# Kernel optimization log

Hardware: AMD Instinct MI355X
Metric: run time of the kernel (lower is better)

Reference implementation:

```python
import jax, jax.numpy as jnp
import numpy as np

NUM_HEADS = 12

def _attn(q, k, v, scale):
    # q,k,v: [..., L, hd]; softmax attention over L (key axis)
    s = jnp.einsum('...qd,...kd->...qk', q, k) * scale
    a = jax.nn.softmax(s, axis=-1)
    return jnp.einsum('...qk,...kd->...qd', a, v)

def setup_inputs() -> dict:
    key = jax.random.key(0)
    k1, k2, k3 = jax.random.split(key, 3)
    B, N, C, D = 8, 256, 16, 768
    x = jax.random.normal(k1, (B, N, C, D), dtype=jnp.float32)
    w_qkv = jax.random.normal(k2, (D, 6 * D), dtype=jnp.float32) * (D ** -0.5)
    w_proj = jax.random.normal(k3, (D, D), dtype=jnp.float32) * (D ** -0.5)
    b_proj = jnp.zeros((D,), dtype=jnp.float32)
    return {"x": x, "w_qkv": w_qkv, "w_proj": w_proj, "b_proj": b_proj}

def reference(x, w_qkv, w_proj, b_proj):
    B, N, C, D = x.shape
    H = NUM_HEADS
    hd = D // H
    scale = hd ** -0.5
    # qkv: [B,N,C,6,H,hd] -> [6,B,H,N,C,hd]
    qkv = (x @ w_qkv).reshape(B, N, C, 6, H, hd).transpose(3, 0, 4, 1, 2, 5)
    qc, kc, qs, ks, vc, vs = qkv[0], qkv[1], qkv[2], qkv[3], qkv[4], qkv[5]
    # spatial attention over N (per channel c): move to [B,H,C,N,hd]
    qs = jnp.swapaxes(qs, -2, -3)
    ks = jnp.swapaxes(ks, -2, -3)
    vs = jnp.swapaxes(vs, -2, -3)
    xs = _attn(qs, ks, vs, scale)          # [B,H,C,N,hd]
    xs = jnp.swapaxes(xs, -2, -3)          # [B,H,N,C,hd]
    # channel attention over C (per token n)
    xc = _attn(qc, kc, vc, scale)          # [B,H,N,C,hd]
    out = xs * xc                           # elementwise combine (fused path)
    # matches torch: x.transpose(1,2).reshape(B,N,C,D)
    out = out.transpose(0, 2, 1, 3, 4).reshape(B, N, C, D)
    return out @ w_proj + b_proj
```

## Files before the change

### kernel.cpp

```cpp
#include <hip/hip_runtime.h>

typedef _Float16 f16;
typedef f16  f16x8 __attribute__((ext_vector_type(8)));
typedef float f32x4 __attribute__((ext_vector_type(4)));

#define S3 3145728LL

__device__ __forceinline__ f32x4 mm(f16x8 a, f16x8 b, f32x4 c) {
  return __builtin_amdgcn_mfma_f32_16x16x32_f16(a, b, c, 0, 0, 0);
}
__device__ __forceinline__ void BAR() { asm volatile("s_barrier" ::: "memory"); }

__device__ __forceinline__ int esw(int t, int col) {
  return t * 128 + ((((col >> 3) ^ ((t ^ (t >> 3)) & 7)) << 3) | (col & 7));
}
__device__ __forceinline__ int oesw(int t, int col) {
  return t * 64 + ((((col >> 3) ^ (t & 7)) << 3) | (col & 7));
}

__global__ void cvt_T_kernel(const float* __restrict__ in, f16* __restrict__ out,
                             int R, int Cc) {
  __shared__ float tile[32][33];
  int tc = blockIdx.x, tr = blockIdx.y;
  int lr = threadIdx.x & 31, lw = threadIdx.x >> 5;
  int c0 = tc * 32, r0 = tr * 32;
#pragma unroll
  for (int i = 0; i < 4; i++)
    tile[lw + 8 * i][lr] = in[(size_t)(r0 + lw + 8 * i) * Cc + c0 + lr];
  __syncthreads();
#pragma unroll
  for (int i = 0; i < 4; i++)
    out[(size_t)(c0 + lw + 8 * i) * R + r0 + lr] = (f16)tile[lr][lw + 8 * i];
}

__global__ void cvt_x_kernel(const float* __restrict__ in, f16* __restrict__ out) {
  size_t i = ((size_t)blockIdx.x * 256 + threadIdx.x) * 8;
  f32x4 a = __builtin_nontemporal_load((const f32x4*)(in + i));
  f32x4 b = __builtin_nontemporal_load((const f32x4*)(in + i + 4));
  f16x8 o;
#pragma unroll
  for (int j = 0; j < 4; j++) { o[j] = (f16)a[j]; o[4 + j] = (f16)b[j]; }
  *(f16x8*)(out + i) = o;
}

#define QST_A(c, q, kt) __builtin_amdgcn_global_load_lds( \
    (const __attribute__((address_space(1))) void*)(aSrc + (size_t)(q) * 24576 + (size_t)(kt) * 64), \
    (__attribute__((address_space(3))) void*)((char*)lds + (c) * 32768 + (q) * 1024 * 4 + wave * 1024), 16, 0, 0)
#define QST_B(c, q, kt) __builtin_amdgcn_global_load_lds( \
    (const __attribute__((address_space(1))) void*)(bSrc + (size_t)(q) * 24576 + (size_t)(kt) * 64), \
    (__attribute__((address_space(3))) void*)((char*)lds + 16384 + (c) * 32768 + (q) * 1024 * 4 + wave * 1024), 16, 0, 0)

__global__ __launch_bounds__(256, 2) void gemm_qkvT(
    const f16* __restrict__ A, const f16* __restrict__ Bt,
    f16* __restrict__ area, long long cstr_) {
  __shared__ f16 lds[32768];
  size_t cstr = (size_t)cstr_;
  int id  = blockIdx.x;
  int cpx = gridDim.x >> 3;
  int id2 = (id & 7) * cpx + (id >> 3);
  int sr = id2 / 288, rr = id2 % 288;
  int bm = sr * 8 + (rr & 7), bn = rr >> 3;

  int tid = threadIdx.x;
  int wave = tid >> 6, lane = tid & 63;
  int l16 = lane & 15, lq = lane >> 4;
  int wr = wave >> 1, wc = wave & 1;
  int l7 = l16 & 7;
  int cb0 = ((lq) ^ l7) << 4;
  int cb1 = ((4 + lq) ^ l7) << 4;

  const f16* aSrc = A  + (size_t)(bm * 128 + (tid >> 3)) * 768 +
                    (((tid & 7) ^ ((tid >> 3) & 7)) << 3);
  const f16* bSrc = Bt + (size_t)(bn * 128 + (tid >> 3)) * 768 +
                    (((tid & 7) ^ ((tid >> 3) & 7)) << 3);

  f32x4 zz = {0.f, 0.f, 0.f, 0.f};
  f32x4 acc[4][4];
#pragma unroll
  for (int m = 0; m < 4; m++)
#pragma unroll
    for (int n = 0; n < 4; n++) acc[m][n] = zz;

#pragma unroll
  for (int q = 0; q < 4; q++) { QST_A(0, q, 0); }
#pragma unroll
  for (int q = 0; q < 4; q++) { QST_B(0, q, 0); }
#pragma unroll
  for (int q = 0; q < 4; q++) { QST_A(1, q, 1); }
#pragma unroll
  for (int q = 0; q < 4; q++) { QST_B(1, q, 1); }
  asm volatile("s_waitcnt vmcnt(8)" ::: "memory");
  BAR();

  f16x8 af[4][2], bf[4][2];
#pragma unroll 2
  for (int t = 0; t < 12; ++t) {
    int c = t & 1;
    const char* ab = (const char*)lds + c * 32768;
    const char* bb = ab + 16384;
    int rA = wr * 64 + l16;
    int rB = wc * 64 + l16;
#pragma unroll
    for (int mf = 0; mf < 4; mf++) {
      af[mf][0] = *(const f16x8*)(ab + (rA + mf * 16) * 128 + cb0);
      af[mf][1] = *(const f16x8*)(ab + (rA + mf * 16) * 128 + cb1);
    }
#pragma unroll
    for (int nf = 0; nf < 4; nf++) {
      bf[nf][0] = *(const f16x8*)(bb + (rB + nf * 16) * 128 + cb0);
      bf[nf][1] = *(const f16x8*)(bb + (rB + nf * 16) * 128 + cb1);
    }
    asm volatile("s_waitcnt lgkmcnt(0)" ::: "memory");
    BAR();
    if (t < 10) {
#pragma unroll
      for (int q = 0; q < 4; q++) { QST_A(c, q, t + 2); }
#pragma unroll
      for (int q = 0; q < 4; q++) { QST_B(c, q, t + 2); }
    }
    __builtin_amdgcn_s_setprio(1);
#pragma unroll
    for (int ks = 0; ks < 2; ks++)
#pragma unroll
      for (int mf = 0; mf < 4; mf++)
#pragma unroll
        for (int nf = 0; nf < 4; nf++)
          acc[mf][nf] = mm(af[mf][ks], bf[nf][ks], acc[mf][nf]);
    __builtin_amdgcn_s_setprio(0);
    if (t < 10) asm volatile("s_waitcnt vmcnt(8)" ::: "memory");
    else        asm volatile("s_waitcnt vmcnt(0)" ::: "memory");
    BAR();
  }

  int s  = bn / 6;
  int h0 = (bn % 6) * 2;
  size_t comp;
  if (s == 0) comp = 0; else if (s == 1) comp = 1; else if (s == 2) comp = 3;
  else if (s == 3) comp = 4; else if (s == 4) comp = 2; else comp = 5;
  int g = (bm * 128) >> 12;
  size_t base = comp * cstr + (size_t)g * S3;
  int n0 = (bm & 31) * 8;

  __syncthreads();
#pragma unroll
  for (int mi = 0; mi < 4; mi++)
#pragma unroll
    for (int ni = 0; ni < 4; ni++)
#pragma unroll
      for (int r = 0; r < 4; r++) {
        int t = wr * 64 + mi * 16 + lq * 4 + r;
        int col = wc * 64 + ni * 16 + l16;
        lds[esw(t, col)] = (f16)acc[mi][ni][r];
      }
  __syncthreads();

  if (s < 2) {
#pragma unroll
    for (int i = 0; i < 4; i++) {
      int u = wave * 4 + i;
      int hl = u >> 3, j16 = u & 7;
#pragma unroll
      for (int half = 0; half < 2; half++) {
        int e0 = half * 512 + lane * 8;
        int cc = e0 >> 6, d0 = e0 & 63;
        f16x8 v = *(const f16x8*)&lds[esw(j16 * 16 + cc, hl * 64 + d0)];
        __builtin_nontemporal_store(v, (f16x8*)&area[base +
            (size_t)(h0 + hl) * 262144 + (size_t)(n0 + j16) * 1024 + e0]);
      }
    }
  } else if (s < 4) {
#pragma unroll
    for (int i = 0; i < 8; i++) {
      int u = wave * 8 + i;
      int hl = u >> 4, cc = u & 15;
      int e = lane * 8;
      int nl = e >> 6, d0 = e & 63;
      f16x8 v = *(const f16x8*)&lds[esw(nl * 16 + cc, hl * 64 + d0)];
      __builtin_nontemporal_store(v, (f16x8*)&area[base +
          (size_t)((h0 + hl) * 16 + cc) * 16384 + (size_t)n0 * 64 + e]);
    }
  } else if (s == 4) {
#pragma unroll
    for (int i = 0; i < 4; i++) {
      int u = wave * 4 + i;
      int hl = u >> 3, j8 = u & 7;
#pragma unroll
      for (int half = 0; half < 2; half++) {
        int e0 = half * 512 + lane * 8;
        int d0 = e0 >> 4, cb = e0 & 15;
        f16x8 v;
#pragma unroll
        for (int j = 0; j < 8; j++)
          v[j] = lds[esw(j8 * 16 + cb + j, hl * 64 + d0)];
        __builtin_nontemporal_store(v, (f16x8*)&area[base +
            (size_t)((h0 + hl) * 256 + n0 + j8) * 1024 + e0]);
      }
    }
  } else {
#pragma unroll
    for (int i = 0; i < 8; i++) {
      int u = wave * 8 + i;
      int hl = u >> 4, cc = u & 15;
      int e = lane * 8;
      int d0 = e >> 3;
      f16x8 v;
#pragma unroll
      for (int j = 0; j < 8; j++)
        v[j] = lds[esw(j * 16 + cc, hl * 64 + d0)];
      __builtin_nontemporal_store(v, (f16x8*)&area[base +
          ((size_t)((h0 + hl) * 16 + cc) * 32 + (bm & 31)) * 512 + e]);
    }
  }
}

__global__ __launch_bounds__(256, 2) void gemm_projT(
    const f16* __restrict__ A,
    const f16* __restrict__ Bt,
    const float* __restrict__ bias, float* __restrict__ Cout) {
  __shared__ f16 lds[32768];
  int id  = blockIdx.x;
  int cpx = gridDim.x >> 3;
  int id2 = (id & 7) * cpx + (id >> 3);
  int sr = id2 / 48, rr = id2 % 48;
  int bm = sr * 8 + (rr & 7), bn = rr >> 3;

  int tid = threadIdx.x;
  int wave = tid >> 6, lane = tid & 63;
  int l16 = lane & 15, lq = lane >> 4;
  int wr = wave >> 1, wc = wave & 1;
  int l7 = l16 & 7;
  int cb0 = ((lq) ^ l7) << 4;
  int cb1 = ((4 + lq) ^ l7) << 4;

  const f16* aSrc = A  + (size_t)(bm * 128 + (tid >> 3)) * 768 +
                    (((tid & 7) ^ ((tid >> 3) & 7)) << 3);
  const f16* bSrc = Bt + (size_t)(bn * 128 + (tid >> 3)) * 768 +
                    (((tid & 7) ^ ((tid >> 3) & 7)) << 3);

  f32x4 zz = {0.f, 0.f, 0.f, 0.f};
  f32x4 acc[4][4];
#pragma unroll
  for (int m = 0; m < 4; m++)
#pragma unroll
    for (int n = 0; n < 4; n++) acc[m][n] = zz;

#pragma unroll
  for (int q = 0; q < 4; q++) { QST_A(0, q, 0); }
#pragma unroll
  for (int q = 0; q < 4; q++) { QST_B(0, q, 0); }
#pragma unroll
  for (int q = 0; q < 4; q++) { QST_A(1, q, 1); }
#pragma unroll
  for (int q = 0; q < 4; q++) { QST_B(1, q, 1); }
  asm volatile("s_waitcnt vmcnt(8)" ::: "memory");
  BAR();

  f16x8 af[4][2], bf[4][2];
#pragma unroll 2
  for (int t = 0; t < 12; ++t) {
    int c = t & 1;
    const char* ab = (const char*)lds + c * 32768;
    const char* bb = ab + 16384;
    int rA = wr * 64 + l16;
    int rB = wc * 64 + l16;
#pragma unroll
    for (int mf = 0; mf < 4; mf++) {
      af[mf][0] = *(const f16x8*)(ab + (rA + mf * 16) * 128 + cb0);
      af[mf][1] = *(const f16x8*)(ab + (rA + mf * 16) * 128 + cb1);
    }
#pragma unroll
    for (int nf = 0; nf < 4; nf++) {
      bf[nf][0] = *(const f16x8*)(bb + (rB + nf * 16) * 128 + cb0);
      bf[nf][1] = *(const f16x8*)(bb + (rB + nf * 16) * 128 + cb1);
    }
    asm volatile("s_waitcnt lgkmcnt(0)" ::: "memory");
    BAR();
    if (t < 10) {
#pragma unroll
      for (int q = 0; q < 4; q++) { QST_A(c, q, t + 2); }
#pragma unroll
      for (int q = 0; q < 4; q++) { QST_B(c, q, t + 2); }
    }
    __builtin_amdgcn_s_setprio(1);
#pragma unroll
    for (int ks = 0; ks < 2; ks++)
#pragma unroll
      for (int mf = 0; mf < 4; mf++)
#pragma unroll
        for (int nf = 0; nf < 4; nf++)
          acc[mf][nf] = mm(af[mf][ks], bf[nf][ks], acc[mf][nf]);
    __builtin_amdgcn_s_setprio(0);
    if (t < 10) asm volatile("s_waitcnt vmcnt(8)" ::: "memory");
    else        asm volatile("s_waitcnt vmcnt(0)" ::: "memory");
    BAR();
  }

#pragma unroll
  for (int ni = 0; ni < 4; ni++) {
    int col = bn * 128 + wc * 64 + ni * 16 + l16;
    float bb = bias[col];
#pragma unroll
    for (int mi = 0; mi < 4; mi++) {
#pragma unroll
      for (int r = 0; r < 4; r++) {
        int row = bm * 128 + wr * 64 + mi * 16 + lq * 4 + r;
        __builtin_nontemporal_store(acc[mi][ni][r] + bb,
                                    &Cout[(size_t)row * 768 + col]);
      }
    }
  }
}

__global__ __launch_bounds__(512) void attn_spat_kernel(f16* __restrict__ area,
                                                        long long cstr_) {
  size_t cstr = (size_t)cstr_;
  int blk = blockIdx.x;
  int g = blk / 192, rem = blk % 192;
  int h = rem >> 4, c = rem & 15;
  size_t goff = (size_t)g * S3;
  const f16* qs = area + 3 * cstr + goff + (size_t)((h * 16 + c) * 256) * 64;
  const f16* ks = area + 4 * cstr + goff + (size_t)((h * 16 + c) * 256) * 64;
  const f16* vsb = area + 5 * cstr + goff + (size_t)(h * 16 + c) * 16384;
  f16* xsn = area + 6 * cstr + goff;

  int tid = threadIdx.x;
  int wave = tid >> 6, lane = tid & 63;
  int l16 = lane & 15, lq = lane >> 4;
  __shared__ f16 plds[8][32][40];
  __shared__ f16 osm[16384];

  f32x4 zz = {0.f, 0.f, 0.f, 0.f};
  f16x8 aq[2][2];
#pragma unroll
  for (int m = 0; m < 2; m++)
#pragma unroll
    for (int kd = 0; kd < 2; kd++)
      aq[m][kd] = *(const f16x8*)&qs[(size_t)(wave * 32 + m * 16 + l16) * 64 + kd * 32 + lq * 8];

  f32x4 o[2][4];
  float mrow[2][4], lrow[2][4];
#pragma unroll
  for (int m = 0; m < 2; m++) {
#pragma unroll
    for (int n = 0; n < 4; n++) o[m][n] = zz;
#pragma unroll
    for (int r = 0; r < 4; r++) { mrow[m][r] = -1e30f; lrow[m][r] = 0.f; }
  }

  for (int kc = 0; kc < 8; kc++) {
    int k0 = kc * 32;
    f16x8 bk00 = *(const f16x8*)&ks[(size_t)(k0 + l16) * 64 + lq * 8];
    f16x8 bk01 = *(const f16x8*)&ks[(size_t)(k0 + l16) * 64 + 32 + lq * 8];
    f16x8 bk10 = *(const f16x8*)&ks[(size_t)(k0 + 16 + l16) * 64 + lq * 8];
    f16x8 bk11 = *(const f16x8*)&ks[(size_t)(k0 + 16 + l16) * 64 + 32 + lq * 8];
    f32x4 st[2][2];
#pragma unroll
    for (int m = 0; m < 2; m++) {
      st[m][0] = mm(aq[m][1], bk01, mm(aq[m][0], bk00, zz));
      st[m][1] = mm(aq[m][1], bk11, mm(aq[m][0], bk10, zz));
    }
#pragma unroll
    for (int m = 0; m < 2; m++) {
#pragma unroll
      for (int r = 0; r < 4; r++) {
        float s0 = st[m][0][r] * 0.125f, s1 = st[m][1][r] * 0.125f;
        float t = fmaxf(s0, s1);
        t = fmaxf(t, __shfl_xor(t, 1));
        t = fmaxf(t, __shfl_xor(t, 2));
        t = fmaxf(t, __shfl_xor(t, 4));
        t = fmaxf(t, __shfl_xor(t, 8));
        float mold = mrow[m][r];
        float mnew = fmaxf(mold, t);
        float fac  = __expf(mold - mnew);
        mrow[m][r] = mnew;
        float p0 = __expf(s0 - mnew), p1 = __expf(s1 - mnew);
        lrow[m][r] = lrow[m][r] * fac + p0 + p1;
        o[m][0][r] *= fac; o[m][1][r] *= fac; o[m][2][r] *= fac; o[m][3][r] *= fac;
        int prow = m * 16 + lq * 4 + r;
        plds[wave][prow][l16]      = (f16)p0;
        plds[wave][prow][16 + l16] = (f16)p1;
      }
    }
    f16x8 ap0 = *(const f16x8*)&plds[wave][l16][lq * 8];
    f16x8 ap1 = *(const f16x8*)&plds[wave][16 + l16][lq * 8];
#pragma unroll
    for (int n = 0; n < 4; n++) {
      f16x8 bv = *(const f16x8*)&vsb[((k0 >> 3) + lq) * 512 + (n * 16 + l16) * 8];
      o[0][n] = mm(ap0, bv, o[0][n]);
      o[1][n] = mm(ap1, bv, o[1][n]);
    }
  }
#pragma unroll
  for (int m = 0; m < 2; m++)
#pragma unroll
    for (int r = 0; r < 4; r++) {
      float l = lrow[m][r];
      l += __shfl_xor(l, 1);
      l += __shfl_xor(l, 2);
      l += __shfl_xor(l, 4);
      l += __shfl_xor(l, 8);
      lrow[m][r] = 1.0f / l;
    }
#pragma unroll
  for (int m = 0; m < 2; m++)
#pragma unroll
    for (int n = 0; n < 4; n++)
#pragma unroll
      for (int r = 0; r < 4; r++) {
        int row = wave * 32 + m * 16 + lq * 4 + r;
        osm[oesw(row, n * 16 + l16)] = (f16)(o[m][n][r] * lrow[m][r]);
      }
  __syncthreads();
  size_t hc64 = (size_t)(h * 16 + c) * 64;
#pragma unroll
  for (int i = 0; i < 4; i++) {
    int row = i * 64 + (tid >> 3);
    int dp  = (tid & 7) * 8;
    f16x8 v = *(const f16x8*)&osm[oesw(row, dp)];
    __builtin_nontemporal_store(v, (f16x8*)&xsn[(size_t)row * 12288 + hc64 + dp]);
  }
}

__global__ __launch_bounds__(256) void attn_chan_kernel(f16* __restrict__ area,
                                                        long long cstr_) {
  size_t cstr = (size_t)cstr_;
  int blk = blockIdx.x;
  int g = blk >> 8, n = blk & 255;
  size_t goff = (size_t)g * S3;
  int tid = threadIdx.x;
  int wave = tid >> 6, lane = tid & 63;
  int l16 = lane & 15, lq = lane >> 4;
  __shared__ f16 xsl[12288];
  __shared__ f16 prl[12288];
  __shared__ f16 plds[4][16][40];

  const f16* xsn = area + 6 * cstr + goff + (size_t)n * 12288;
#pragma unroll
  for (int i = 0; i < 6; i++) {
    int seg = wave * 6 + i;
    __builtin_amdgcn_global_load_lds(
        (const __attribute__((address_space(1))) void*)(xsn + seg * 512 + lane * 8),
        (__attribute__((address_space(3))) void*)((char*)xsl + seg * 1024), 16, 0, 0);
  }
  if (lane < 16) {
#pragma unroll
    for (int j = 0; j < 16; j++) plds[wave][lane][16 + j] = (f16)0.f;
  }
  asm volatile("s_waitcnt vmcnt(0)" ::: "memory");
  __syncthreads();

  f32x4 zz = {0.f, 0.f, 0.f, 0.f};
  for (int hi = 0; hi < 3; hi++) {
    int h = wave + hi * 4;
    const f16* q = area + 0 * cstr + goff + (size_t)((h * 256 + n) * 16) * 64;
    const f16* k = area + 1 * cstr + goff + (size_t)((h * 256 + n) * 16) * 64;
    const f16* v = area + 2 * cstr + goff + (size_t)((h * 256 + n) * 64) * 16;
    f16x8 a0 = *(const f16x8*)&q[l16 * 64 + lq * 8];
    f16x8 a1 = *(const f16x8*)&q[l16 * 64 + 32 + lq * 8];
    f16x8 b0 = *(const f16x8*)&k[l16 * 64 + lq * 8];
    f16x8 b1 = *(const f16x8*)&k[l16 * 64 + 32 + lq * 8];
    f32x4 s = mm(a1, b1, mm(a0, b0, zz));
    float p[4];
#pragma unroll
    for (int r = 0; r < 4; r++) {
      float t = s[r] * 0.125f;
      float mx = t;
      mx = fmaxf(mx, __shfl_xor(mx, 1));
      mx = fmaxf(mx, __shfl_xor(mx, 2));
      mx = fmaxf(mx, __shfl_xor(mx, 4));
      mx = fmaxf(mx, __shfl_xor(mx, 8));
      float e = __expf(t - mx);
      float sum = e;
      sum += __shfl_xor(sum, 1);
      sum += __shfl_xor(sum, 2);
      sum += __shfl_xor(sum, 4);
      sum += __shfl_xor(sum, 8);
      p[r] = e / sum;
    }
#pragma unroll
    for (int r = 0; r < 4; r++)
      plds[wave][lq * 4 + r][l16] = (f16)p[r];
    f16x8 ap = *(const f16x8*)&plds[wave][l16][lq * 8];
#pragma unroll
    for (int nt = 0; nt < 4; nt++) {
      f16x8 bv = *(const f16x8*)&v[(nt * 16 + l16) * 16 + lq * 8];
      f32x4 o = mm(ap, bv, zz);
#pragma unroll
      for (int r = 0; r < 4; r++) {
        int cq = lq * 4 + r, d = nt * 16 + l16;
        int idx = h * 1024 + cq * 64 + d;
        float xsv = (float)xsl[idx];
        prl[idx] = (f16)(o[r] * xsv);
      }
    }
  }
  __syncthreads();
  f16* prod = area + 3 * cstr + goff + (size_t)n * 12288;
#pragma unroll
  for (int i = 0; i < 6; i++) {
    f16x8 v = *(const f16x8*)&prl[i * 2048 + tid * 8];
    __builtin_nontemporal_store(v, (f16x8*)&prod[i * 2048 + tid * 8]);
  }
}

extern "C" void kernel_launch(void* const* d_in, const int* in_sizes, int n_in,
                              void* d_out, int out_size, void* d_ws, size_t ws_size,
                              hipStream_t stream) {
  const float* x      = (const float*)d_in[0];
  const float* w_qkv  = (const float*)d_in[1];
  const float* w_proj = (const float*)d_in[2];
  const float* b_proj = (const float*)d_in[3];
  float* out = (float*)d_out;
  f16* ws = (f16*)d_ws;

  const size_t W16T = 4608ull * 768;
  const size_t WPT  = 768ull * 768;
  f16* w16t = ws;
  f16* wpt  = ws + W16T;
  f16* area = wpt + WPT;

  int G = 8;
  while (G > 1 && (W16T + WPT + 7ull * G * S3) * 2 > ws_size) G >>= 1;
  int nch = 8 / G;
  long long cstr = (long long)G * S3;
  f16* x16 = area + 6 * (size_t)cstr;

  cvt_T_kernel<<<dim3(144, 24), 256, 0, stream>>>(w_qkv, w16t, 768, 4608);
  cvt_T_kernel<<<dim3(24, 24), 256, 0, stream>>>(w_proj, wpt, 768, 768);

  for (int ch = 0; ch < nch; ch++) {
    size_t b0 = (size_t)ch * G;
    cvt_x_kernel<<<G * 1536, 256, 0, stream>>>(x + b0 * S3, x16);
    gemm_qkvT<<<G * 1152, 256, 0, stream>>>(x16, w16t, area, cstr);
    attn_spat_kernel<<<G * 192, 512, 0, stream>>>(area, cstr);
    attn_chan_kernel<<<G * 256, 256, 0, stream>>>(area, cstr);
    gemm_projT<<<G * 192, 256, 0, stream>>>(area + 3 * (size_t)cstr, wpt, b_proj,
                                            out + b0 * S3);
  }
}
```

Baseline: 508.2 us.

## Replace QKV GEMM with 256x256-tile, 8-wave, four-phase pipelined kernel

The QKV projection GEMM moves from 128x128 tiles with 4 waves to 256x256 tiles with 8 waves and 128 KB of LDS double buffering. The K-loop is split into four MFMA phases, and the global-to-LDS loads for the next stages are interleaved between them. The aim is more reuse of each loaded tile and better overlap of loads with MFMA work. The scatter epilogue is unified for the larger tile, at the cost of fewer workgroups and more LDS and register pressure per block.

Result: no change. 504.1 us (-0.8%).

```diff
diff --git a/kernel.cpp b/kernel.cpp
--- a/kernel.cpp
+++ b/kernel.cpp
@@ -10,9 +10,11 @@
   return __builtin_amdgcn_mfma_f32_16x16x32_f16(a, b, c, 0, 0, 0);
 }
 __device__ __forceinline__ void BAR() { asm volatile("s_barrier" ::: "memory"); }
-
-__device__ __forceinline__ int esw(int t, int col) {
-  return t * 128 + ((((col >> 3) ^ ((t ^ (t >> 3)) & 7)) << 3) | (col & 7));
+#define LGKM0() do { asm volatile("s_waitcnt lgkmcnt(0)" ::: "memory"); \
+                     __builtin_amdgcn_sched_barrier(0); } while (0)
+
+__device__ __forceinline__ int esw256(int t, int col) {
+  return t * 256 + ((((col >> 3) ^ ((t ^ (t >> 3)) & 7)) << 3) | (col & 7));
 }
 __device__ __forceinline__ int oesw(int t, int col) {
   return t * 64 + ((((col >> 3) ^ (t & 7)) << 3) | (col & 7));
@@ -43,6 +45,193 @@
   *(f16x8*)(out + i) = o;
 }
 
+#define P8_A(c, q, kt) __builtin_amdgcn_global_load_lds( \
+    (const __attribute__((address_space(1))) void*)(aSrc + (size_t)(q) * 49152 + (size_t)(kt) * 64), \
+    (__attribute__((address_space(3))) void*)((char*)lds + (c) * 65536 + (q) * 8192 + tid * 16), 16, 0, 0)
+#define P8_B(c, q, kt) __builtin_amdgcn_global_load_lds( \
+    (const __attribute__((address_space(1))) void*)(bSrc + (size_t)(q) * 49152 + (size_t)(kt) * 64), \
+    (__attribute__((address_space(3))) void*)((char*)lds + (c) * 65536 + 32768 + (q) * 8192 + tid * 16), 16, 0, 0)
+
+__global__ __launch_bounds__(512, 2) void gemm_qkv8p(
+    const f16* __restrict__ A, const f16* __restrict__ Bt,
+    f16* __restrict__ area, long long cstr_) {
+  __shared__ f16 lds[65536];
+  size_t cstr = (size_t)cstr_;
+  int id  = blockIdx.x;
+  int cpx = gridDim.x >> 3;
+  int id2 = (id & 7) * cpx + (id >> 3);
+  int sr = id2 / 144, rr = id2 % 144;
+  int bm = sr * 8 + (rr & 7), bn = rr >> 3;
+
+  int tid = threadIdx.x;
+  int wave = tid >> 6, lane = tid & 63;
+  int l16 = lane & 15, lq = lane >> 4;
+  int wr = wave >> 2, wc = wave & 3;
+  int l7 = l16 & 7;
+  int cb0 = ((lq) ^ l7) << 4;
+  int cb1 = ((4 + lq) ^ l7) << 4;
+
+  const f16* aSrc = A  + (size_t)(bm * 256 + (tid >> 3)) * 768 +
+                    (((tid & 7) ^ ((tid >> 3) & 7)) << 3);
+  const f16* bSrc = Bt + (size_t)(bn * 256 + (tid >> 3)) * 768 +
+                    (((tid & 7) ^ ((tid >> 3) & 7)) << 3);
+
+  f32x4 zz = {0.f, 0.f, 0.f, 0.f};
+  f32x4 acc[8][4];
+#pragma unroll
+  for (int m = 0; m < 8; m++)
+#pragma unroll
+    for (int n = 0; n < 4; n++) acc[m][n] = zz;
+
+  P8_A(0, 0, 0); P8_A(0, 1, 0); P8_A(0, 2, 0); P8_A(0, 3, 0);
+  P8_B(0, 0, 0); P8_B(0, 1, 0); P8_B(0, 2, 0); P8_B(0, 3, 0);
+  P8_A(1, 0, 1); P8_A(1, 2, 1);
+  P8_B(1, 0, 1); P8_B(1, 1, 1); P8_B(1, 2, 1); P8_B(1, 3, 1);
+  asm volatile("s_waitcnt vmcnt(6)" ::: "memory");
+  BAR();
+
+  f16x8 af[4][2], ag[4][2], b01[2][2], b23[2][2];
+#pragma unroll 2
+  for (int t = 0; t < 12; ++t) {
+    int c = t & 1, o = c ^ 1;
+    const char* ab = (const char*)lds + c * 65536;
+    const char* bb = ab + 32768;
+    int rA = wr * 128 + l16;
+    int rB = wc * 64 + l16;
+
+#pragma unroll
+    for (int mf = 0; mf < 4; mf++) {
+      af[mf][0] = *(const f16x8*)(ab + (rA + mf * 16) * 128 + cb0);
+      af[mf][1] = *(const f16x8*)(ab + (rA + mf * 16) * 128 + cb1);
+    }
+#pragma unroll
+    for (int nf = 0; nf < 2; nf++) {
+      b01[nf][0] = *(const f16x8*)(bb + (rB + nf * 16) * 128 + cb0);
+      b01[nf][1] = *(const f16x8*)(bb + (rB + nf * 16) * 128 + cb1);
+    }
+    if (t < 11) { P8_A(o, 1, t + 1); P8_A(o, 3, t + 1); }
+    BAR(); LGKM0();
+    __builtin_amdgcn_s_setprio(1);
+#pragma unroll
+    for (int ks = 0; ks < 2; ks++)
+#pragma unroll
+      for (int mf = 0; mf < 4; mf++)
+#pragma unroll
+        for (int nf = 0; nf < 2; nf++)
+          acc[mf][nf] = mm(af[mf][ks], b01[nf][ks], acc[mf][nf]);
+    __builtin_amdgcn_s_setprio(0);
+    BAR();
+
+#pragma unroll
+    for (int nf = 0; nf < 2; nf++) {
+      b23[nf][0] = *(const f16x8*)(bb + (rB + 32 + nf * 16) * 128 + cb0);
+      b23[nf][1] = *(const f16x8*)(bb + (rB + 32 + nf * 16) * 128 + cb1);
+    }
+    if (t < 10) { P8_A(c, 0, t + 2); P8_A(c, 2, t + 2); }
+    BAR(); LGKM0();
+    __builtin_amdgcn_s_setprio(1);
+#pragma unroll
+    for (int ks = 0; ks < 2; ks++)
+#pragma unroll
+      for (int mf = 0; mf < 4; mf++)
+#pragma unroll
+        for (int nf = 0; nf < 2; nf++)
+          acc[mf][2 + nf] = mm(af[mf][ks], b23[nf][ks], acc[mf][2 + nf]);
+    __builtin_amdgcn_s_setprio(0);
+    BAR();
+
+#pragma unroll
+    for (int mf = 0; mf < 4; mf++) {
+      ag[mf][0] = *(const f16x8*)(ab + (rA + 64 + mf * 16) * 128 + cb0);
+      ag[mf][1] = *(const f16x8*)(ab + (rA + 64 + mf * 16) * 128 + cb1);
+    }
+    if (t < 10) { P8_B(c, 0, t + 2); P8_B(c, 1, t + 2); }
+    BAR(); LGKM0();
+    __builtin_amdgcn_s_setprio(1);
+#pragma unroll
+    for (int ks = 0; ks < 2; ks++)
+#pragma unroll
+      for (int mf = 0; mf < 4; mf++)
+#pragma unroll
+        for (int nf = 0; nf < 2; nf++)
+          acc[4 + mf][nf] = mm(ag[mf][ks], b01[nf][ks], acc[4 + mf][nf]);
+    __builtin_amdgcn_s_setprio(0);
+    BAR();
+
+    if (t < 10) { P8_B(c, 2, t + 2); P8_B(c, 3, t + 2); }
+    __builtin_amdgcn_s_setprio(1);
+#pragma unroll
+    for (int ks = 0; ks < 2; ks++)
+#pragma unroll
+      for (int mf = 0; mf < 4; mf++)
+#pragma unroll
+        for (int nf = 0; nf < 2; nf++)
+          acc[4 + mf][2 + nf] = mm(ag[mf][ks], b23[nf][ks], acc[4 + mf][2 + nf]);
+    __builtin_amdgcn_s_setprio(0);
+    if (t < 10) asm volatile("s_waitcnt vmcnt(6)" ::: "memory");
+    else        asm volatile("s_waitcnt vmcnt(0)" ::: "memory");
+    BAR();
+  }
+
+  int s  = bn / 3;
+  int h0 = (bn % 3) * 4;
+  size_t comp;
+  if (s == 0) comp = 0; else if (s == 1) comp = 1; else if (s == 2) comp = 3;
+  else if (s == 3) comp = 4; else if (s == 4) comp = 2; else comp = 5;
+  int g = bm >> 4;
+  size_t base = comp * cstr + (size_t)g * S3;
+  int n0 = (bm & 15) * 16;
+
+  __syncthreads();
+#pragma unroll
+  for (int mi = 0; mi < 8; mi++)
+#pragma unroll
+    for (int ni = 0; ni < 4; ni++)
+#pragma unroll
+      for (int r = 0; r < 4; r++) {
+        int tl = wr * 128 + (mi >> 2) * 64 + (mi & 3) * 16 + lq * 4 + r;
+        int col = wc * 64 + ni * 16 + l16;
+        lds[esw256(tl, col)] = (f16)acc[mi][ni][r];
+      }
+  __syncthreads();
+
+#pragma unroll
+  for (int i = 0; i < 8; i++) {
+    int u = wave * 8 + i;
+    int hl = u >> 4, j16 = u & 15;
+    int h  = h0 + hl;
+#pragma unroll
+    for (int half = 0; half < 2; half++) {
+      int e0 = half * 512 + lane * 8;
+      f16x8 v;
+      size_t dst;
+      if (s < 2) {
+        int cc = e0 >> 6, d0 = e0 & 63;
+        v = *(const f16x8*)&lds[esw256(j16 * 16 + cc, hl * 64 + d0)];
+        dst = base + (size_t)h * 262144 + (size_t)(n0 + j16) * 1024 + e0;
+      } else if (s < 4) {
+        int nl = e0 >> 6, d0 = e0 & 63;
+        v = *(const f16x8*)&lds[esw256(nl * 16 + j16, hl * 64 + d0)];
+        dst = base + (size_t)(h * 16 + j16) * 16384 + (size_t)n0 * 64 + e0;
+      } else if (s == 4) {
+        int d0 = e0 >> 4, cb = e0 & 15;
+#pragma unroll
+        for (int j = 0; j < 8; j++)
+          v[j] = lds[esw256(j16 * 16 + cb + j, hl * 64 + d0)];
+        dst = base + (size_t)(h * 256 + n0 + j16) * 1024 + e0;
+      } else {
+        int d0 = (e0 >> 3) & 63, nbl = e0 >> 9;
+#pragma unroll
+        for (int j = 0; j < 8; j++)
+          v[j] = lds[esw256((nbl * 8 + j) * 16 + j16, hl * 64 + d0)];
+        dst = base + ((size_t)(h * 16 + j16) * 32 + (n0 >> 3) + nbl) * 512 +
+              (e0 & 511);
+      }
+      __builtin_nontemporal_store(v, (f16x8*)&area[dst]);
+    }
+  }
+}
+
 #define QST_A(c, q, kt) __builtin_amdgcn_global_load_lds( \
     (const __attribute__((address_space(1))) void*)(aSrc + (size_t)(q) * 24576 + (size_t)(kt) * 64), \
     (__attribute__((address_space(3))) void*)((char*)lds + (c) * 32768 + (q) * 1024 * 4 + wave * 1024), 16, 0, 0)
@@ -50,172 +239,8 @@
     (const __attribute__((address_space(1))) void*)(bSrc + (size_t)(q) * 24576 + (size_t)(kt) * 64), \
     (__attribute__((address_space(3))) void*)((char*)lds + 16384 + (c) * 32768 + (q) * 1024 * 4 + wave * 1024), 16, 0, 0)
 
-__global__ __launch_bounds__(256, 2) void gemm_qkvT(
+__global__ __launch_bounds__(256, 2) void gemm_projT(
     const f16* __restrict__ A, const f16* __restrict__ Bt,
-    f16* __restrict__ area, long long cstr_) {
-  __shared__ f16 lds[32768];
-  size_t cstr = (size_t)cstr_;
-  int id  = blockIdx.x;
-  int cpx = gridDim.x >> 3;
-  int id2 = (id & 7) * cpx + (id >> 3);
-  int sr = id2 / 288, rr = id2 % 288;
-  int bm = sr * 8 + (rr & 7), bn = rr >> 3;
-
-  int tid = threadIdx.x;
-  int wave = tid >> 6, lane = tid & 63;
-  int l16 = lane & 15, lq = lane >> 4;
-  int wr = wave >> 1, wc = wave & 1;
-  int l7 = l16 & 7;
-  int cb0 = ((lq) ^ l7) << 4;
-  int cb1 = ((4 + lq) ^ l7) << 4;
-
-  const f16* aSrc = A  + (size_t)(bm * 128 + (tid >> 3)) * 768 +
-                    (((tid & 7) ^ ((tid >> 3) & 7)) << 3);
-  const f16* bSrc = Bt + (size_t)(bn * 128 + (tid >> 3)) * 768 +
-                    (((tid & 7) ^ ((tid >> 3) & 7)) << 3);
-
-  f32x4 zz = {0.f, 0.f, 0.f, 0.f};
-  f32x4 acc[4][4];
-#pragma unroll
-  for (int m = 0; m < 4; m++)
-#pragma unroll
-    for (int n = 0; n < 4; n++) acc[m][n] = zz;
-
-#pragma unroll
-  for (int q = 0; q < 4; q++) { QST_A(0, q, 0); }
-#pragma unroll
-  for (int q = 0; q < 4; q++) { QST_B(0, q, 0); }
-#pragma unroll
-  for (int q = 0; q < 4; q++) { QST_A(1, q, 1); }
-#pragma unroll
-  for (int q = 0; q < 4; q++) { QST_B(1, q, 1); }
-  asm volatile("s_waitcnt vmcnt(8)" ::: "memory");
-  BAR();
-
-  f16x8 af[4][2], bf[4][2];
-#pragma unroll 2
-  for (int t = 0; t < 12; ++t) {
-    int c = t & 1;
-    const char* ab = (const char*)lds + c * 32768;
-    const char* bb = ab + 16384;
-    int rA = wr * 64 + l16;
-    int rB = wc * 64 + l16;
-#pragma unroll
-    for (int mf = 0; mf < 4; mf++) {
-      af[mf][0] = *(const f16x8*)(ab + (rA + mf * 16) * 128 + cb0);
-      af[mf][1] = *(const f16x8*)(ab + (rA + mf * 16) * 128 + cb1);
-    }
-#pragma unroll
-    for (int nf = 0; nf < 4; nf++) {
-      bf[nf][0] = *(const f16x8*)(bb + (rB + nf * 16) * 128 + cb0);
-      bf[nf][1] = *(const f16x8*)(bb + (rB + nf * 16) * 128 + cb1);
-    }
-    asm volatile("s_waitcnt lgkmcnt(0)" ::: "memory");
-    BAR();
-    if (t < 10) {
-#pragma unroll
-      for (int q = 0; q < 4; q++) { QST_A(c, q, t + 2); }
-#pragma unroll
-      for (int q = 0; q < 4; q++) { QST_B(c, q, t + 2); }
-    }
-    __builtin_amdgcn_s_setprio(1);
-#pragma unroll
-    for (int ks = 0; ks < 2; ks++)
-#pragma unroll
-      for (int mf = 0; mf < 4; mf++)
-#pragma unroll
-        for (int nf = 0; nf < 4; nf++)
-          acc[mf][nf] = mm(af[mf][ks], bf[nf][ks], acc[mf][nf]);
-    __builtin_amdgcn_s_setprio(0);
-    if (t < 10) asm volatile("s_waitcnt vmcnt(8)" ::: "memory");
-    else        asm volatile("s_waitcnt vmcnt(0)" ::: "memory");
-    BAR();
-  }
-
-  int s  = bn / 6;
-  int h0 = (bn % 6) * 2;
-  size_t comp;
-  if (s == 0) comp = 0; else if (s == 1) comp = 1; else if (s == 2) comp = 3;
-  else if (s == 3) comp = 4; else if (s == 4) comp = 2; else comp = 5;
-  int g = (bm * 128) >> 12;
-  size_t base = comp * cstr + (size_t)g * S3;
-  int n0 = (bm & 31) * 8;
-
-  __syncthreads();
-#pragma unroll
-  for (int mi = 0; mi < 4; mi++)
-#pragma unroll
-    for (int ni = 0; ni < 4; ni++)
-#pragma unroll
-      for (int r = 0; r < 4; r++) {
-        int t = wr * 64 + mi * 16 + lq * 4 + r;
-        int col = wc * 64 + ni * 16 + l16;
-        lds[esw(t, col)] = (f16)acc[mi][ni][r];
-      }
-  __syncthreads();
-
-  if (s < 2) {
-#pragma unroll
-    for (int i = 0; i < 4; i++) {
-      int u = wave * 4 + i;
-      int hl = u >> 3, j16 = u & 7;
-#pragma unroll
-      for (int half = 0; half < 2; half++) {
-        int e0 = half * 512 + lane * 8;
-        int cc = e0 >> 6, d0 = e0 & 63;
-        f16x8 v = *(const f16x8*)&lds[esw(j16 * 16 + cc, hl * 64 + d0)];
-        __builtin_nontemporal_store(v, (f16x8*)&area[base +
-            (size_t)(h0 + hl) * 262144 + (size_t)(n0 + j16) * 1024 + e0]);
-      }
-    }
-  } else if (s < 4) {
-#pragma unroll
-    for (int i = 0; i < 8; i++) {
-      int u = wave * 8 + i;
-      int hl = u >> 4, cc = u & 15;
-      int e = lane * 8;
-      int nl = e >> 6, d0 = e & 63;
-      f16x8 v = *(const f16x8*)&lds[esw(nl * 16 + cc, hl * 64 + d0)];
-      __builtin_nontemporal_store(v, (f16x8*)&area[base +
-          (size_t)((h0 + hl) * 16 + cc) * 16384 + (size_t)n0 * 64 + e]);
-    }
-  } else if (s == 4) {
-#pragma unroll
-    for (int i = 0; i < 4; i++) {
-      int u = wave * 4 + i;
-      int hl = u >> 3, j8 = u & 7;
-#pragma unroll
-      for (int half = 0; half < 2; half++) {
-        int e0 = half * 512 + lane * 8;
-        int d0 = e0 >> 4, cb = e0 & 15;
-        f16x8 v;
-#pragma unroll
-        for (int j = 0; j < 8; j++)
-          v[j] = lds[esw(j8 * 16 + cb + j, hl * 64 + d0)];
-        __builtin_nontemporal_store(v, (f16x8*)&area[base +
-            (size_t)((h0 + hl) * 256 + n0 + j8) * 1024 + e0]);
-      }
-    }
-  } else {
-#pragma unroll
-    for (int i = 0; i < 8; i++) {
-      int u = wave * 8 + i;
-      int hl = u >> 4, cc = u & 15;
-      int e = lane * 8;
-      int d0 = e >> 3;
-      f16x8 v;
-#pragma unroll
-      for (int j = 0; j < 8; j++)
-        v[j] = lds[esw(j * 16 + cc, hl * 64 + d0)];
-      __builtin_nontemporal_store(v, (f16x8*)&area[base +
-          ((size_t)((h0 + hl) * 16 + cc) * 32 + (bm & 31)) * 512 + e]);
-    }
-  }
-}
-
-__global__ __launch_bounds__(256, 2) void gemm_projT(
-    const f16* __restrict__ A,
-    const f16* __restrict__ Bt,
     const float* __restrict__ bias, float* __restrict__ Cout) {
   __shared__ f16 lds[32768];
   int id  = blockIdx.x;
@@ -531,7 +556,7 @@
   for (int ch = 0; ch < nch; ch++) {
     size_t b0 = (size_t)ch * G;
     cvt_x_kernel<<<G * 1536, 256, 0, stream>>>(x + b0 * S3, x16);
-    gemm_qkvT<<<G * 1152, 256, 0, stream>>>(x16, w16t, area, cstr);
+    gemm_qkv8p<<<G * 288, 512, 0, stream>>>(x16, w16t, area, cstr);
     attn_spat_kernel<<<G * 192, 512, 0, stream>>>(area, cstr);
     attn_chan_kernel<<<G * 256, 256, 0, stream>>>(area, cstr);
     gemm_projT<<<G * 192, 256, 0, stream>>>(area + 3 * (size_t)cstr, wpt, b_proj,
```
